# Kernel tuning notes

Measured on AMD Instinct MI355X. Metric: run time of the kernel, lower is better.

## Reference

```python
import jax, jax.numpy as jnp
import numpy as np


def setup_inputs() -> dict:
    key = jax.random.key(0)
    k1, k2 = jax.random.split(key)
    z = jax.random.normal(k1, (128, 784, 256), dtype=jnp.float32)
    codebook = jax.random.normal(k2, (1024, 256), dtype=jnp.float32)
    return {"z": z, "codebook": codebook}


def reference(z, codebook):
    # z: [b, t, d]; codebook: [K, d]
    b, t, d = z.shape
    zf = z.reshape(b * t, d)                              # (b t) d
    # pairwise squared distances: ||z||^2 + ||c||^2 - 2 z.c
    dist = (
        jnp.sum(zf * zf, axis=1, keepdims=True)
        + jnp.sum(codebook * codebook, axis=1)
        - 2.0 * jnp.einsum("nd,kd->nk", zf, codebook)
    )                                                      # (b t) K
    min_idx = jnp.argmin(dist, axis=1)                     # (b t)
    z_q = codebook[min_idx]                                # (b t) d  gather
    b_min_idx = min_idx.reshape(b, t)
    sg = jax.lax.stop_gradient
    loss_vq = jnp.mean((z_q - sg(zf)) ** 2)
    loss_commit = jnp.mean((zf - sg(z_q)) ** 2)
    z_q_st = zf + sg(z_q - zf)                             # straight-through
    z_q_st = z_q_st.reshape(b, t, d)
    return (loss_vq, loss_commit, z_q_st, b_min_idx)
```

## Files before the change

### kernel.cpp

```cpp
#include <hip/hip_runtime.h>
#include <hip/hip_bf16.h>

typedef float  f32x4  __attribute__((ext_vector_type(4)));
typedef short  short4v __attribute__((ext_vector_type(4)));
typedef short  short8v __attribute__((ext_vector_type(8)));

#define DIM   256
#define BM    128
#define BN    128
#define NTM   256
#define EPS   0.05f
#define RB    2048
#define GB    1024

__device__ __forceinline__ ushort bf16rn(float f) {
  union { float f; uint u; } x; x.f = f;
  const uint u = x.u;
  return (ushort)((u + 0x7fffu + ((u >> 16) & 1u)) >> 16);
}
__device__ __forceinline__ float bf16tof(ushort h) {
  union { uint u; float f; } x; x.u = ((uint)h) << 16; return x.f;
}

__global__ __launch_bounds__(64) void vq_cnorm(const float* __restrict__ cb,
                                               double* __restrict__ cn2,
                                               float* __restrict__ cnf) {
  const int k    = blockIdx.x;
  const int lane = threadIdx.x;
  const f32x4 v = ((const f32x4*)(cb + (size_t)k * DIM))[lane];
  double s = (double)v[0]*v[0] + (double)v[1]*v[1] +
             (double)v[2]*v[2] + (double)v[3]*v[3];
  for (int off = 32; off; off >>= 1) s += __shfl_down(s, off, 64);
  if (lane == 0) { cn2[k] = s; cnf[k] = (float)s; }
}

__global__ __launch_bounds__(NTM, 2) void vq_mfma(const float* __restrict__ z,
                                                  const float* __restrict__ cb,
                                                  const float* __restrict__ cnf,
                                                  float* __restrict__ idx_out) {
  __shared__ __align__(16) ushort zhS[BM*64];
  __shared__ __align__(16) ushort zlS[BM*64];
  __shared__ __align__(16) ushort chS[BN*64];
  __shared__ __align__(16) ushort clS[BN*64];
  __shared__ float cns[1024];
  __shared__ float rb1[2][BM];
  __shared__ float rb2[2][BM];
  __shared__ int   ri1[2][BM];

  char* zhB = (char*)zhS; char* zlB = (char*)zlS;
  char* chB = (char*)chS; char* clB = (char*)clS;

  const int t  = threadIdx.x;
  const int l  = t & 63, w = t >> 6;
  const int wm = w >> 1, wn = w & 1;
  const int lr = l & 15, lg = l >> 4;
  const size_t rbase = (size_t)blockIdx.x * BM;
  const uint rswz = (uint)(lr & 7) << 4;

  for (int i = t; i < 1024; i += NTM) cns[i] = cnf[i];

  float b1[16], b2[16]; int i1[16];
  #pragma unroll
  for (int s = 0; s < 16; ++s) { b1[s] = 3.0e38f; b2[s] = 3.0e38f; i1[s] = 0; }

  const int kq = t & 15, r2 = t >> 4;
  const f32x4* zg4 = (const f32x4*)z;
  const f32x4* cg4 = (const f32x4*)cb;

  for (int chunk = 0; chunk < 8; ++chunk) {
    f32x4 acc[4][4];
    #pragma unroll
    for (int m = 0; m < 4; ++m)
      #pragma unroll
      for (int n = 0; n < 4; ++n) acc[m][n] = (f32x4){0.f, 0.f, 0.f, 0.f};

    for (int kt = 0; kt < 4; ++kt) {
      __syncthreads();
      #pragma unroll
      for (int j = 0; j < 8; ++j) {
        const int r = r2 + j*16;
        const f32x4 vz = zg4[(rbase + r)*64 + kt*16 + kq];
        const f32x4 vc = cg4[((size_t)(chunk*BN + r))*64 + kt*16 + kq];
        short4v hz, lz, hc, lc;
        #pragma unroll
        for (int e = 0; e < 4; ++e) {
          const float fz = vz[e];
          const ushort hb = bf16rn(fz);
          hz[e] = (short)hb;
          lz[e] = (short)bf16rn(fz - bf16tof(hb));
          const float fc = vc[e];
          const ushort hb2 = bf16rn(fc);
          hc[e] = (short)hb2;
          lc[e] = (short)bf16rn(fc - bf16tof(hb2));
        }
        const uint off = ((uint)(r*128 + kq*8)) ^ ((uint)(r & 7) << 4);
        *(short4v*)(zhB + off) = hz;
        *(short4v*)(zlB + off) = lz;
        *(short4v*)(chB + off) = hc;
        *(short4v*)(clB + off) = lc;
      }
      __syncthreads();
      #pragma unroll
      for (int kk = 0; kk < 2; ++kk) {
        short8v ah[4], al_[4], bh[4], bl_[4];
        #pragma unroll
        for (int m = 0; m < 4; ++m) {
          const int r = wm*64 + m*16 + lr;
          const uint off = ((uint)(r*128 + kk*64 + lg*16)) ^ rswz;
          ah[m]  = *(const short8v*)(zhB + off);
          al_[m] = *(const short8v*)(zlB + off);
        }
        #pragma unroll
        for (int n = 0; n < 4; ++n) {
          const int r = wn*64 + n*16 + lr;
          const uint off = ((uint)(r*128 + kk*64 + lg*16)) ^ rswz;
          bh[n]  = *(const short8v*)(chB + off);
          bl_[n] = *(const short8v*)(clB + off);
        }
        #pragma unroll
        for (int m = 0; m < 4; ++m)
          #pragma unroll
          for (int n = 0; n < 4; ++n) {
            acc[m][n] = __builtin_amdgcn_mfma_f32_16x16x32_bf16(ah[m],  bh[n],  acc[m][n], 0, 0, 0);
            acc[m][n] = __builtin_amdgcn_mfma_f32_16x16x32_bf16(ah[m],  bl_[n], acc[m][n], 0, 0, 0);
            acc[m][n] = __builtin_amdgcn_mfma_f32_16x16x32_bf16(al_[m], bh[n],  acc[m][n], 0, 0, 0);
          }
      }
    }
    #pragma unroll
    for (int m = 0; m < 4; ++m)
      #pragma unroll
      for (int n = 0; n < 4; ++n) {
        const int cg = chunk*128 + wn*64 + n*16 + lr;
        const float cn = cns[cg & 1023];
        #pragma unroll
        for (int r = 0; r < 4; ++r) {
          const float dd = fmaf(-2.0f, acc[m][n][r], cn);
          const int s = m*4 + r;
          const bool lt = dd < b1[s];
          b2[s] = lt ? b1[s] : fminf(b2[s], dd);
          i1[s] = lt ? cg : i1[s];
          b1[s] = lt ? dd : b1[s];
        }
      }
  }

  #pragma unroll
  for (int s = 0; s < 16; ++s) {
    #pragma unroll
    for (int off = 1; off < 16; off <<= 1) {
      const float ob1 = __shfl_xor(b1[s], off, 16);
      const float ob2 = __shfl_xor(b2[s], off, 16);
      const int   oi  = __shfl_xor(i1[s], off, 16);
      const float hi  = fmaxf(b1[s], ob1);
      b2[s] = fminf(fminf(b2[s], ob2), hi);
      if (ob1 < b1[s] || (ob1 == b1[s] && oi < i1[s])) { b1[s] = ob1; i1[s] = oi; }
    }
  }
  if (lr == 0) {
    #pragma unroll
    for (int m = 0; m < 4; ++m)
      #pragma unroll
      for (int r = 0; r < 4; ++r) {
        const int s = m*4 + r;
        const int row = wm*64 + m*16 + lg*4 + r;
        rb1[wn][row] = b1[s]; rb2[wn][row] = b2[s]; ri1[wn][row] = i1[s];
      }
  }
  __syncthreads();
  if (t < BM) {
    const float a1 = rb1[0][t], a2 = rb2[0][t]; const int ai = ri1[0][t];
    const float c1 = rb1[1][t], c2 = rb2[1][t]; const int ci = ri1[1][t];
    const float m2 = fminf(fminf(a2, c2), fmaxf(a1, c1));
    float m1; int mi;
    if (c1 < a1 || (c1 == a1 && ci < ai)) { m1 = c1; mi = ci; } else { m1 = a1; mi = ai; }
    idx_out[rbase + t] = (m2 - m1 > EPS) ? (float)mi : -1.0f;
  }
}

__global__ __launch_bounds__(256) void vq_recheck(const float* __restrict__ z,
                                                  const float* __restrict__ cb,
                                                  const double* __restrict__ cn2,
                                                  float* __restrict__ idx_out, int N) {
  __shared__ __align__(16) float zrow[DIM];
  __shared__ __align__(16) float cbs[32*DIM];
  __shared__ double bls[32];
  __shared__ int    bis[32];
  const int t = threadIdx.x;
  for (int row = blockIdx.x; row < N; row += RB) {
    const float f = idx_out[row];
    if (f >= 0.0f) continue;
    if (t < 64) ((f32x4*)zrow)[t] = ((const f32x4*)z)[(size_t)row*64 + t];
    double best = 1.0e300; int bidx = 0;
    for (int ch = 0; ch < 32; ++ch) {
      __syncthreads();
      #pragma unroll
      for (int i = 0; i < 8; ++i)
        ((f32x4*)cbs)[t + i*256] = ((const f32x4*)cb)[(size_t)ch*2048 + t + i*256];
      __syncthreads();
      const float* cr = cbs  + (t >> 3)*DIM + (t & 7)*32;
      const float* zr = zrow + (t & 7)*32;
      double s = 0.0;
      #pragma unroll
      for (int d = 0; d < 32; ++d) s = fma((double)zr[d], (double)cr[d], s);
      s += __shfl_xor(s, 4, 8);
      s += __shfl_xor(s, 2, 8);
      s += __shfl_xor(s, 1, 8);
      if ((t & 7) == 0) {
        const int code = ch*32 + (t >> 3);
        const double dd = cn2[code] - 2.0*s;
        if (dd < best) { best = dd; bidx = code; }
      }
    }
    __syncthreads();
    if ((t & 7) == 0) { bls[t >> 3] = best; bis[t >> 3] = bidx; }
    __syncthreads();
    if (t == 0) {
      double bb = bls[0]; int ii = bis[0];
      for (int q = 1; q < 32; ++q)
        if (bls[q] < bb || (bls[q] == bb && bis[q] < ii)) { bb = bls[q]; ii = bis[q]; }
      idx_out[row] = (float)ii;
    }
    __syncthreads();
  }
}

__global__ __launch_bounds__(256) void vq_gather(const float* __restrict__ z,
                                                 const float* __restrict__ cb,
                                                 const float* __restrict__ idxf,
                                                 float* __restrict__ zq,
                                                 double* __restrict__ loss_acc, int N) {
  const int t = threadIdx.x, wid = t >> 6, lane = t & 63;
  double ls = 0.0;
  for (int row = blockIdx.x*4 + wid; row < N; row += GB*4) {
    const int idx = (int)idxf[row];
    const f32x4 q  = ((const f32x4*)cb)[(size_t)idx*64 + lane];
    const f32x4 zz = ((const f32x4*)z)[(size_t)row*64 + lane];
    ((f32x4*)zq)[(size_t)row*64 + lane] = q;
    const double dx = (double)q[0] - (double)zz[0];
    const double dy = (double)q[1] - (double)zz[1];
    const double dz2 = (double)q[2] - (double)zz[2];
    const double dw = (double)q[3] - (double)zz[3];
    ls += dx*dx + dy*dy + dz2*dz2 + dw*dw;
  }
  #pragma unroll
  for (int off = 32; off; off >>= 1) ls += __shfl_down(ls, off, 64);
  __shared__ double wsum[4];
  if (lane == 0) wsum[wid] = ls;
  __syncthreads();
  if (t == 0) atomicAdd(loss_acc, wsum[0] + wsum[1] + wsum[2] + wsum[3]);
}

__global__ void vq_finalize(const double* __restrict__ loss_acc,
                            float* __restrict__ out, double inv) {
  const float l = (float)(loss_acc[0] * inv);
  out[0] = l;
  out[1] = l;
}

extern "C" void kernel_launch(void* const* d_in, const int* in_sizes, int n_in,
                              void* d_out, int out_size, void* d_ws, size_t ws_size,
                              hipStream_t stream) {
  const float* z  = (const float*)d_in[0];
  const float* cb = (const float*)d_in[1];
  const int N = in_sizes[0] / DIM;
  const int K = in_sizes[1] / DIM;
  (void)K;

  float* out     = (float*)d_out;
  float* zq_out  = out + 2;
  float* idx_out = out + 2 + (size_t)N * DIM;

  double* loss_acc = (double*)d_ws;
  double* cn2      = (double*)((char*)d_ws + 64);
  float*  cnf      = (float*)((char*)d_ws + 64 + 8192);

  hipMemsetAsync(d_ws, 0, 64, stream);
  vq_cnorm<<<1024, 64, 0, stream>>>(cb, cn2, cnf);
  vq_mfma<<<N / BM, NTM, 0, stream>>>(z, cb, cnf, idx_out);
  vq_recheck<<<RB, 256, 0, stream>>>(z, cb, cn2, idx_out, N);
  vq_gather<<<GB, 256, 0, stream>>>(z, cb, idx_out, zq_out, loss_acc, N);
  vq_finalize<<<1, 1, 0, stream>>>(loss_acc, out, 1.0 / ((double)N * (double)DIM));
}
```

Before: 808.4 us.

## Precompute bf16 hi/lo codebook once and stream it from global in MFMA kernel

The codebook bf16 hi/lo split now happens once in the norm kernel and is written to workspace, so it is no longer recomputed by every block. The MFMA kernel keeps a full 64-row z tile (hi/lo, all 256 dims) resident in LDS, converted once, and reads codebook fragments straight from global/L2 without per-k-step LDS staging or barriers. The row tile drops from 128 to 64, doubling the grid, and B-operand reuse across waves now depends on L2 and cache hits rather than shared memory.

```diff
diff --git a/kernel.cpp b/kernel.cpp
--- a/kernel.cpp
+++ b/kernel.cpp
@@ -6,9 +6,8 @@
 typedef short  short8v __attribute__((ext_vector_type(8)));
 
 #define DIM   256
-#define BM    128
-#define BN    128
-#define NTM   256
+#define BM2   64
+#define NT2   256
 #define EPS   0.05f
 #define RB    2048
 #define GB    1024
@@ -24,129 +23,129 @@
 
 __global__ __launch_bounds__(64) void vq_cnorm(const float* __restrict__ cb,
                                                double* __restrict__ cn2,
-                                               float* __restrict__ cnf) {
+                                               float* __restrict__ cnf,
+                                               ushort* __restrict__ cbh,
+                                               ushort* __restrict__ cbl) {
   const int k    = blockIdx.x;
   const int lane = threadIdx.x;
   const f32x4 v = ((const f32x4*)(cb + (size_t)k * DIM))[lane];
+  short4v h, lo;
+  #pragma unroll
+  for (int e = 0; e < 4; ++e) {
+    const ushort hb = bf16rn(v[e]);
+    h[e]  = (short)hb;
+    lo[e] = (short)bf16rn(v[e] - bf16tof(hb));
+  }
+  *(short4v*)(cbh + (size_t)k * DIM + lane * 4) = h;
+  *(short4v*)(cbl + (size_t)k * DIM + lane * 4) = lo;
   double s = (double)v[0]*v[0] + (double)v[1]*v[1] +
              (double)v[2]*v[2] + (double)v[3]*v[3];
   for (int off = 32; off; off >>= 1) s += __shfl_down(s, off, 64);
   if (lane == 0) { cn2[k] = s; cnf[k] = (float)s; }
 }
 
-__global__ __launch_bounds__(NTM, 2) void vq_mfma(const float* __restrict__ z,
-                                                  const float* __restrict__ cb,
-                                                  const float* __restrict__ cnf,
-                                                  float* __restrict__ idx_out) {
-  __shared__ __align__(16) ushort zhS[BM*64];
-  __shared__ __align__(16) ushort zlS[BM*64];
-  __shared__ __align__(16) ushort chS[BN*64];
-  __shared__ __align__(16) ushort clS[BN*64];
+__global__ __launch_bounds__(NT2, 2) void vq_mfma2(const float* __restrict__ z,
+                                                   const ushort* __restrict__ cbh,
+                                                   const ushort* __restrict__ cbl,
+                                                   const float* __restrict__ cnf,
+                                                   float* __restrict__ idx_out) {
+  __shared__ __align__(16) ushort zhS[BM2 * DIM];
+  __shared__ __align__(16) ushort zlS[BM2 * DIM];
   __shared__ float cns[1024];
-  __shared__ float rb1[2][BM];
-  __shared__ float rb2[2][BM];
-  __shared__ int   ri1[2][BM];
+  __shared__ float rb1[2][BM2];
+  __shared__ float rb2[2][BM2];
+  __shared__ int   ri1[2][BM2];
 
   char* zhB = (char*)zhS; char* zlB = (char*)zlS;
-  char* chB = (char*)chS; char* clB = (char*)clS;
+  const char* cbhB = (const char*)cbh;
+  const char* cblB = (const char*)cbl;
 
   const int t  = threadIdx.x;
   const int l  = t & 63, w = t >> 6;
   const int wm = w >> 1, wn = w & 1;
   const int lr = l & 15, lg = l >> 4;
-  const size_t rbase = (size_t)blockIdx.x * BM;
-  const uint rswz = (uint)(lr & 7) << 4;
-
-  for (int i = t; i < 1024; i += NTM) cns[i] = cnf[i];
-
-  float b1[16], b2[16]; int i1[16];
-  #pragma unroll
-  for (int s = 0; s < 16; ++s) { b1[s] = 3.0e38f; b2[s] = 3.0e38f; i1[s] = 0; }
-
-  const int kq = t & 15, r2 = t >> 4;
-  const f32x4* zg4 = (const f32x4*)z;
-  const f32x4* cg4 = (const f32x4*)cb;
+  const size_t rbase = (size_t)blockIdx.x * BM2;
+
+  for (int i = t; i < 1024; i += NT2) cns[i] = cnf[i];
+
+  {
+    const f32x4* zg4 = (const f32x4*)z;
+    for (int i = t; i < BM2 * 64; i += NT2) {
+      const int r = i >> 6, c = i & 63;
+      const f32x4 vz = zg4[(rbase + r) * 64 + c];
+      short4v hz, lz;
+      #pragma unroll
+      for (int e = 0; e < 4; ++e) {
+        const ushort hb = bf16rn(vz[e]);
+        hz[e] = (short)hb;
+        lz[e] = (short)bf16rn(vz[e] - bf16tof(hb));
+      }
+      const uint off = ((uint)(r * 512 + c * 8)) ^ ((uint)(r & 7) << 4);
+      *(short4v*)(zhB + off) = hz;
+      *(short4v*)(zlB + off) = lz;
+    }
+  }
+  __syncthreads();
+
+  float b1[8], b2[8]; int i1[8];
+  #pragma unroll
+  for (int s = 0; s < 8; ++s) { b1[s] = 3.0e38f; b2[s] = 3.0e38f; i1[s] = 0; }
 
   for (int chunk = 0; chunk < 8; ++chunk) {
-    f32x4 acc[4][4];
-    #pragma unroll
-    for (int m = 0; m < 4; ++m)
+    f32x4 acc[2][4];
+    #pragma unroll
+    for (int m = 0; m < 2; ++m)
       #pragma unroll
       for (int n = 0; n < 4; ++n) acc[m][n] = (f32x4){0.f, 0.f, 0.f, 0.f};
 
-    for (int kt = 0; kt < 4; ++kt) {
-      __syncthreads();
-      #pragma unroll
-      for (int j = 0; j < 8; ++j) {
-        const int r = r2 + j*16;
-        const f32x4 vz = zg4[(rbase + r)*64 + kt*16 + kq];
-        const f32x4 vc = cg4[((size_t)(chunk*BN + r))*64 + kt*16 + kq];
-        short4v hz, lz, hc, lc;
-        #pragma unroll
-        for (int e = 0; e < 4; ++e) {
-          const float fz = vz[e];
-          const ushort hb = bf16rn(fz);
-          hz[e] = (short)hb;
-          lz[e] = (short)bf16rn(fz - bf16tof(hb));
-          const float fc = vc[e];
-          const ushort hb2 = bf16rn(fc);
-          hc[e] = (short)hb2;
-          lc[e] = (short)bf16rn(fc - bf16tof(hb2));
-        }
-        const uint off = ((uint)(r*128 + kq*8)) ^ ((uint)(r & 7) << 4);
-        *(short4v*)(zhB + off) = hz;
-        *(short4v*)(zlB + off) = lz;
-        *(short4v*)(chB + off) = hc;
-        *(short4v*)(clB + off) = lc;
-      }
-      __syncthreads();
-      #pragma unroll
-      for (int kk = 0; kk < 2; ++kk) {
-        short8v ah[4], al_[4], bh[4], bl_[4];
-        #pragma unroll
-        for (int m = 0; m < 4; ++m) {
-          const int r = wm*64 + m*16 + lr;
-          const uint off = ((uint)(r*128 + kk*64 + lg*16)) ^ rswz;
-          ah[m]  = *(const short8v*)(zhB + off);
-          al_[m] = *(const short8v*)(zlB + off);
-        }
+    #pragma unroll
+    for (int s = 0; s < 8; ++s) {
+      short8v ah[2], al_[2];
+      #pragma unroll
+      for (int m = 0; m < 2; ++m) {
+        const int r = wm * 32 + m * 16 + lr;
+        const uint off = ((uint)(r * 512 + s * 64 + lg * 16)) ^ ((uint)(r & 7) << 4);
+        ah[m]  = *(const short8v*)(zhB + off);
+        al_[m] = *(const short8v*)(zlB + off);
+      }
+      short8v bh[4], bl_[4];
+      #pragma unroll
+      for (int n = 0; n < 4; ++n) {
+        const uint code = (uint)(chunk * 128 + wn * 64 + n * 16 + lr);
+        const uint goff = code * 512 + (uint)(s * 64 + lg * 16);
+        bh[n]  = *(const short8v*)(cbhB + goff);
+        bl_[n] = *(const short8v*)(cblB + goff);
+      }
+      #pragma unroll
+      for (int m = 0; m < 2; ++m)
         #pragma unroll
         for (int n = 0; n < 4; ++n) {
-          const int r = wn*64 + n*16 + lr;
-          const uint off = ((uint)(r*128 + kk*64 + lg*16)) ^ rswz;
-          bh[n]  = *(const short8v*)(chB + off);
-          bl_[n] = *(const short8v*)(clB + off);
+          acc[m][n] = __builtin_amdgcn_mfma_f32_16x16x32_bf16(ah[m],  bh[n],  acc[m][n], 0, 0, 0);
+          acc[m][n] = __builtin_amdgcn_mfma_f32_16x16x32_bf16(ah[m],  bl_[n], acc[m][n], 0, 0, 0);
+          acc[m][n] = __builtin_amdgcn_mfma_f32_16x16x32_bf16(al_[m], bh[n],  acc[m][n], 0, 0, 0);
         }
-        #pragma unroll
-        for (int m = 0; m < 4; ++m)
-          #pragma unroll
-          for (int n = 0; n < 4; ++n) {
-            acc[m][n] = __builtin_amdgcn_mfma_f32_16x16x32_bf16(ah[m],  bh[n],  acc[m][n], 0, 0, 0);
-            acc[m][n] = __builtin_amdgcn_mfma_f32_16x16x32_bf16(ah[m],  bl_[n], acc[m][n], 0, 0, 0);
-            acc[m][n] = __builtin_amdgcn_mfma_f32_16x16x32_bf16(al_[m], bh[n],  acc[m][n], 0, 0, 0);
-          }
-      }
-    }
-    #pragma unroll
-    for (int m = 0; m < 4; ++m)
-      #pragma unroll
-      for (int n = 0; n < 4; ++n) {
-        const int cg = chunk*128 + wn*64 + n*16 + lr;
-        const float cn = cns[cg & 1023];
+    }
+
+    #pragma unroll
+    for (int n = 0; n < 4; ++n) {
+      const int cg = chunk * 128 + wn * 64 + n * 16 + lr;
+      const float cn = cns[cg];
+      #pragma unroll
+      for (int m = 0; m < 2; ++m)
         #pragma unroll
         for (int r = 0; r < 4; ++r) {
           const float dd = fmaf(-2.0f, acc[m][n][r], cn);
-          const int s = m*4 + r;
+          const int s = m * 4 + r;
           const bool lt = dd < b1[s];
           b2[s] = lt ? b1[s] : fminf(b2[s], dd);
           i1[s] = lt ? cg : i1[s];
           b1[s] = lt ? dd : b1[s];
         }
-      }
-  }
-
-  #pragma unroll
-  for (int s = 0; s < 16; ++s) {
+    }
+  }
+
+  #pragma unroll
+  for (int s = 0; s < 8; ++s) {
     #pragma unroll
     for (int off = 1; off < 16; off <<= 1) {
       const float ob1 = __shfl_xor(b1[s], off, 16);
@@ -159,16 +158,16 @@
   }
   if (lr == 0) {
     #pragma unroll
-    for (int m = 0; m < 4; ++m)
+    for (int m = 0; m < 2; ++m)
       #pragma unroll
       for (int r = 0; r < 4; ++r) {
-        const int s = m*4 + r;
-        const int row = wm*64 + m*16 + lg*4 + r;
+        const int s = m * 4 + r;
+        const int row = wm * 32 + m * 16 + lg * 4 + r;
         rb1[wn][row] = b1[s]; rb2[wn][row] = b2[s]; ri1[wn][row] = i1[s];
       }
   }
   __syncthreads();
-  if (t < BM) {
+  if (t < BM2) {
     const float a1 = rb1[0][t], a2 = rb2[0][t]; const int ai = ri1[0][t];
     const float c1 = rb1[1][t], c2 = rb2[1][t]; const int ci = ri1[1][t];
     const float m2 = fminf(fminf(a2, c2), fmaxf(a1, c1));
@@ -274,10 +273,12 @@
   double* loss_acc = (double*)d_ws;
   double* cn2      = (double*)((char*)d_ws + 64);
   float*  cnf      = (float*)((char*)d_ws + 64 + 8192);
+  ushort* cbh      = (ushort*)((char*)d_ws + 64 + 8192 + 4096);
+  ushort* cbl      = (ushort*)((char*)d_ws + 64 + 8192 + 4096 + 524288);
 
   hipMemsetAsync(d_ws, 0, 64, stream);
-  vq_cnorm<<<1024, 64, 0, stream>>>(cb, cn2, cnf);
-  vq_mfma<<<N / BM, NTM, 0, stream>>>(z, cb, cnf, idx_out);
+  vq_cnorm<<<1024, 64, 0, stream>>>(cb, cn2, cnf, cbh, cbl);
+  vq_mfma2<<<N / BM2, NT2, 0, stream>>>(z, cbh, cbl, cnf, idx_out);
   vq_recheck<<<RB, 256, 0, stream>>>(z, cb, cn2, idx_out, N);
   vq_gather<<<GB, 256, 0, stream>>>(z, cb, idx_out, zq_out, loss_acc, N);
   vq_finalize<<<1, 1, 0, stream>>>(loss_acc, out, 1.0 / ((double)N * (double)DIM));
```

Result: slower. 982.4 us (+21.5%).
